# Optimization experiments

Measured on AMD Instinct MI355X. Metric: run time of the kernel, lower is better.

Reference implementation:

```python
import jax, jax.numpy as jnp
import numpy as np

N, S, Q, P = 20000, 400, 20, 3


def setup_inputs() -> dict:
    key = jax.random.key(0)
    k1, k2, k3, k4 = jax.random.split(key, 4)
    # Learned parameters (post-projection state: non-negative, ~L2-normalized)
    heads_param = jax.random.uniform(k1, (S, Q, P), dtype=jnp.float32)
    heads_param = heads_param / jnp.linalg.norm(heads_param, axis=-1, keepdims=True)
    head_ratios_param = jax.random.uniform(k2, (S,), dtype=jnp.float32)
    head_ratios_param = head_ratios_param / jnp.linalg.norm(head_ratios_param)
    # Forward inputs
    batch_pauli_tensor = jax.random.uniform(k3, (N, Q, P), dtype=jnp.float32)
    batch_coeff = jax.random.normal(k4, (N,), dtype=jnp.float32)
    return {
        "heads_param": heads_param,
        "head_ratios_param": head_ratios_param,
        "batch_pauli_tensor": batch_pauli_tensor,
        "batch_coeff": batch_coeff,
    }


def reference(heads_param, head_ratios_param, batch_pauli_tensor, batch_coeff):
    p_exp = 2  # module-level constant `p`
    heads = heads_param ** p_exp              # [s,q,p]
    head_ratios = head_ratios_param ** p_exp  # [s]
    # coverage per (word, head, qubit): dot over Pauli axis
    shadow_coverage = jnp.einsum('nqp,sqp->nsq', batch_pauli_tensor, heads)  # [n,s,q]
    coverage = jnp.prod(shadow_coverage, axis=-1)                            # [n,s]
    coverage = jnp.einsum('s,ns->n', head_ratios, coverage)                  # [n]
    loss_val = jnp.sum((batch_coeff ** 2) / coverage)
    return (loss_val, head_ratios, heads)
```

## Files before the change

### kernel.cpp

```cpp
#include <hip/hip_runtime.h>

#define NN 20000
#define SS 400
#define QQ 20
#define PP 3
#define QP (QQ*PP)
#define NPB 64
#define NBLK ((NN + NPB - 1)/NPB)
#define NPAD (NBLK*NPB)

#define GSPLIT 10
#define SPAIRS (SS/2)
#define SP_PER_BLK (SPAIRS/GSPLIT)
#define WAVES 4
#define BLK_B (WAVES*64)
#define SP_PER_WAVE (SP_PER_BLK/WAVES)

#define WS_H    0
#define WS_R    (SPAIRS*QP*2)
#define WS_COV  (WS_R + SS)
#define WS_PART (WS_COV + GSPLIT*NPAD)
#define CBLK    ((NPAD + 255)/256)

typedef float v2f __attribute__((ext_vector_type(2)));

__device__ __forceinline__ v2f lo4(float4 f) { v2f r; r.x = f.x; r.y = f.y; return r; }
__device__ __forceinline__ v2f hi4(float4 f) { v2f r; r.x = f.z; r.y = f.w; return r; }

__global__ void prep_kernel(const float* __restrict__ heads_param,
                            const float* __restrict__ ratios_param,
                            float* __restrict__ out, float* __restrict__ ws) {
    int i = blockIdx.x * blockDim.x + threadIdx.x;
    if (i < SS*QP) {
        float v = heads_param[i];
        float v2 = v * v;
        out[1 + SS + i] = v2;
        int s = i / QP;
        int k = i - s * QP;
        int sp = s >> 1, j = s & 1;
        ws[WS_H + (sp*QP + k)*2 + j] = v2;
    }
    if (i < SS) {
        float v = ratios_param[i];
        float v2 = v * v;
        out[1 + i] = v2;
        ws[WS_R + i] = v2;
    }
}

#define SP_STEP(ACC, SP)                                                \
    do {                                                                \
        const float4* row4 = lds_h4 + (wbase + (SP))*30 + c*6;          \
        float4 f0 = row4[0], f1 = row4[1], f2 = row4[2];                \
        v2f d0 = lo4(f0)*pqa.x + hi4(f0)*pqa.y + lo4(f1)*pqa.z;         \
        v2f d1 = hi4(f1)*pqa.w + lo4(f2)*pqb.x + hi4(f2)*pqb.y;         \
        float4 f3 = row4[3], f4 = row4[4], f5 = row4[5];                \
        v2f d2 = lo4(f3)*pqb.z + hi4(f3)*pqb.w + lo4(f4)*pqc.x;         \
        v2f d3 = hi4(f4)*pqc.y + lo4(f5)*pqc.z + hi4(f5)*pqc.w;         \
        ACC *= (d0*d1)*(d2*d3);                                         \
    } while (0)

__global__ __launch_bounds__(BLK_B) void main_kernel(
        const float* __restrict__ pauli, float* __restrict__ ws) {
    __shared__ float4 lds_h4[SP_PER_BLK * QP / 2];
    __shared__ float4 lds_r4[SP_PER_BLK * 2 / 4];
    __shared__ float  lds_cov[WAVES][NPB];

    const int tid  = threadIdx.x;
    const int wave = __builtin_amdgcn_readfirstlane(tid >> 6);
    const int lane = tid & 63;
    const int g    = blockIdx.y;
    const int n    = blockIdx.x * NPB + lane;
    const int nc   = (n < NN) ? n : (NN - 1);
    const int wbase = wave * SP_PER_WAVE;

    {
        const float4* srcH = reinterpret_cast<const float4*>(ws + WS_H + (size_t)g * (SP_PER_BLK*QP*2));
        for (int i = tid; i < SP_PER_BLK*QP/2; i += BLK_B) lds_h4[i] = srcH[i];
        const float4* srcR = reinterpret_cast<const float4*>(ws + WS_R + g * (SP_PER_BLK*2));
        if (tid < SP_PER_BLK*2/4) lds_r4[tid] = srcR[tid];
    }

    const float4* p4 = reinterpret_cast<const float4*>(pauli + (size_t)nc * QP);

    __syncthreads();

    v2f a0, a1, a2, a3, a4;
    a0.x=1.f; a0.y=1.f; a1=a0; a2=a0; a3=a0; a4=a0;

    #pragma unroll 1
    for (int c = 0; c < 5; ++c) {
        float4 pqa = p4[c*3+0], pqb = p4[c*3+1], pqc = p4[c*3+2];
        SP_STEP(a0, 0);
        SP_STEP(a1, 1);
        SP_STEP(a2, 2);
        SP_STEP(a3, 3);
        SP_STEP(a4, 4);
    }

    const v2f* r2p = reinterpret_cast<const v2f*>(lds_r4);
    v2f cov2 = r2p[wbase+0]*a0 + r2p[wbase+1]*a1 + r2p[wbase+2]*a2
             + r2p[wbase+3]*a3 + r2p[wbase+4]*a4;

    lds_cov[wave][lane] = cov2.x + cov2.y;
    __syncthreads();

    if (tid < NPB) {
        float cv = 0.f;
        #pragma unroll
        for (int w = 0; w < WAVES; ++w) cv += lds_cov[w][tid];
        ws[WS_COV + (size_t)g * NPAD + blockIdx.x * NPB + tid] = cv;
    }
}

__global__ void combine_kernel(const float* __restrict__ wsc,
                               const float* __restrict__ coeff,
                               float* __restrict__ ws) {
    __shared__ float red[4];
    const int tid = threadIdx.x;
    const int n = blockIdx.x * 256 + tid;
    float term = 0.f;
    if (n < NN) {
        float cov = 0.f;
        #pragma unroll
        for (int g = 0; g < GSPLIT; ++g) cov += wsc[WS_COV + (size_t)g * NPAD + n];
        float c = coeff[n];
        term = (c * c) / cov;
    }
    #pragma unroll
    for (int off = 32; off; off >>= 1) term += __shfl_down(term, off);
    if ((tid & 63) == 0) red[tid >> 6] = term;
    __syncthreads();
    if (tid == 0) ws[WS_PART + blockIdx.x] = red[0] + red[1] + red[2] + red[3];
}

__global__ void final_kernel(const float* __restrict__ ws, float* __restrict__ out) {
    int tid = threadIdx.x;
    double acc = 0.0;
    for (int i = tid; i < CBLK; i += 128) acc += (double)ws[WS_PART + i];
    #pragma unroll
    for (int off = 32; off; off >>= 1) acc += __shfl_down(acc, off);
    __shared__ double r2[2];
    if ((tid & 63) == 0) r2[tid >> 6] = acc;
    __syncthreads();
    if (tid == 0) out[0] = (float)(r2[0] + r2[1]);
}

extern "C" void kernel_launch(void* const* d_in, const int* in_sizes, int n_in,
                              void* d_out, int out_size, void* d_ws, size_t ws_size,
                              hipStream_t stream) {
    const float* heads_param  = (const float*)d_in[0];
    const float* ratios_param = (const float*)d_in[1];
    const float* pauli        = (const float*)d_in[2];
    const float* coeff        = (const float*)d_in[3];
    float* out = (float*)d_out;
    float* ws  = (float*)d_ws;

    prep_kernel<<<(SS*QP + 255)/256, 256, 0, stream>>>(heads_param, ratios_param, out, ws);
    main_kernel<<<dim3(NBLK, GSPLIT), BLK_B, 0, stream>>>(pauli, ws);
    combine_kernel<<<CBLK, 256, 0, stream>>>(ws, coeff, ws);
    final_kernel<<<1, 128, 0, stream>>>(ws, out);
}
```

Measured before the change: 34.82 us.

## Pack word pairs into vector lanes and fold head ratios into heads

The prep kernel now interleaves the Pauli tensor so that each lane processes two words at once as a float2, with heads stored unpacked and read as broadcast scalars. The head ratio is folded into the first qubit's head entries, so the per-head weighting step is replaced by a plain sum. Waves per block are doubled so each wave still covers five heads. The cost is an extra full read and write of the Pauli tensor in the prep kernel, which may outweigh the savings in the main kernel.

```diff
diff --git a/kernel.cpp b/kernel.cpp
--- a/kernel.cpp
+++ b/kernel.cpp
@@ -3,24 +3,23 @@
 #define NN 20000
 #define SS 400
 #define QQ 20
-#define PP 3
-#define QP (QQ*PP)
-#define NPB 64
-#define NBLK ((NN + NPB - 1)/NPB)
-#define NPAD (NBLK*NPB)
-
+#define QP 60
+#define NPAIRS ((NN+1)/2)
+#define JPB 64
+#define NBLK ((NPAIRS + JPB - 1)/JPB)
+#define JPAD (NBLK*JPB)
+#define NP2 (JPAD*2)
 #define GSPLIT 10
-#define SPAIRS (SS/2)
-#define SP_PER_BLK (SPAIRS/GSPLIT)
-#define WAVES 4
+#define SB (SS/GSPLIT)
+#define WAVES 8
 #define BLK_B (WAVES*64)
-#define SP_PER_WAVE (SP_PER_BLK/WAVES)
+#define SW (SB/WAVES)
 
 #define WS_H    0
-#define WS_R    (SPAIRS*QP*2)
-#define WS_COV  (WS_R + SS)
-#define WS_PART (WS_COV + GSPLIT*NPAD)
-#define CBLK    ((NPAD + 255)/256)
+#define WS_P    (SS*QP)
+#define WS_COV  (WS_P + JPAD*QP*2)
+#define WS_PART (WS_COV + GSPLIT*NP2)
+#define CBLK    ((NP2 + 255)/256)
 
 typedef float v2f __attribute__((ext_vector_type(2)));
 
@@ -29,87 +28,85 @@
 
 __global__ void prep_kernel(const float* __restrict__ heads_param,
                             const float* __restrict__ ratios_param,
+                            const float* __restrict__ pauli,
                             float* __restrict__ out, float* __restrict__ ws) {
     int i = blockIdx.x * blockDim.x + threadIdx.x;
+    if (i < NN*QP) {
+        int n = i / QP, k = i - n * QP;
+        int j = n >> 1, b = n & 1;
+        ws[WS_P + j*(QP*2) + k*2 + b] = pauli[i];
+    }
     if (i < SS*QP) {
+        int s = i / QP, k = i - s * QP;
         float v = heads_param[i];
         float v2 = v * v;
         out[1 + SS + i] = v2;
-        int s = i / QP;
-        int k = i - s * QP;
-        int sp = s >> 1, j = s & 1;
-        ws[WS_H + (sp*QP + k)*2 + j] = v2;
+        float r = ratios_param[s];
+        ws[WS_H + i] = (k < 3) ? v2 * (r*r) : v2;
     }
     if (i < SS) {
-        float v = ratios_param[i];
-        float v2 = v * v;
-        out[1 + i] = v2;
-        ws[WS_R + i] = v2;
+        float r = ratios_param[i];
+        out[1 + i] = r * r;
     }
 }
 
-#define SP_STEP(ACC, SP)                                                \
+#define S_STEP(A, S)                                                    \
     do {                                                                \
-        const float4* row4 = lds_h4 + (wbase + (SP))*30 + c*6;          \
-        float4 f0 = row4[0], f1 = row4[1], f2 = row4[2];                \
-        v2f d0 = lo4(f0)*pqa.x + hi4(f0)*pqa.y + lo4(f1)*pqa.z;         \
-        v2f d1 = hi4(f1)*pqa.w + lo4(f2)*pqb.x + hi4(f2)*pqb.y;         \
-        float4 f3 = row4[3], f4 = row4[4], f5 = row4[5];                \
-        v2f d2 = lo4(f3)*pqb.z + hi4(f3)*pqb.w + lo4(f4)*pqc.x;         \
-        v2f d3 = hi4(f4)*pqc.y + lo4(f5)*pqc.z + hi4(f5)*pqc.w;         \
-        ACC *= (d0*d1)*(d2*d3);                                         \
+        const float4* hf = reinterpret_cast<const float4*>(hw + (S)*QP + c*12); \
+        float4 f0 = hf[0], f1 = hf[1], f2 = hf[2];                      \
+        v2f d0 = pq0*f0.x + pq1*f0.y  + pq2*f0.z;                       \
+        v2f d1 = pq3*f0.w + pq4*f1.x  + pq5*f1.y;                       \
+        v2f d2 = pq6*f1.z + pq7*f1.w  + pq8*f2.x;                       \
+        v2f d3 = pq9*f2.y + pq10*f2.z + pq11*f2.w;                      \
+        A *= (d0*d1)*(d2*d3);                                           \
     } while (0)
 
-__global__ __launch_bounds__(BLK_B) void main_kernel(
-        const float* __restrict__ pauli, float* __restrict__ ws) {
-    __shared__ float4 lds_h4[SP_PER_BLK * QP / 2];
-    __shared__ float4 lds_r4[SP_PER_BLK * 2 / 4];
-    __shared__ float  lds_cov[WAVES][NPB];
+__global__ __launch_bounds__(BLK_B) void main_kernel(float* __restrict__ ws) {
+    __shared__ float ldsH[SB*QP];
+    __shared__ v2f   ldsC[WAVES][64];
 
     const int tid  = threadIdx.x;
     const int wave = __builtin_amdgcn_readfirstlane(tid >> 6);
     const int lane = tid & 63;
     const int g    = blockIdx.y;
-    const int n    = blockIdx.x * NPB + lane;
-    const int nc   = (n < NN) ? n : (NN - 1);
-    const int wbase = wave * SP_PER_WAVE;
+    const int j    = blockIdx.x * JPB + lane;
 
     {
-        const float4* srcH = reinterpret_cast<const float4*>(ws + WS_H + (size_t)g * (SP_PER_BLK*QP*2));
-        for (int i = tid; i < SP_PER_BLK*QP/2; i += BLK_B) lds_h4[i] = srcH[i];
-        const float4* srcR = reinterpret_cast<const float4*>(ws + WS_R + g * (SP_PER_BLK*2));
-        if (tid < SP_PER_BLK*2/4) lds_r4[tid] = srcR[tid];
+        const float4* src = reinterpret_cast<const float4*>(ws + WS_H + (size_t)g * (SB*QP));
+        float4* dst = reinterpret_cast<float4*>(ldsH);
+        for (int i = tid; i < SB*QP/4; i += BLK_B) dst[i] = src[i];
     }
-
-    const float4* p4 = reinterpret_cast<const float4*>(pauli + (size_t)nc * QP);
-
     __syncthreads();
 
+    const float4* ppj = reinterpret_cast<const float4*>(ws + WS_P + (size_t)j * (QP*2));
+    const float* hw = ldsH + wave * (SW*QP);
+
     v2f a0, a1, a2, a3, a4;
-    a0.x=1.f; a0.y=1.f; a1=a0; a2=a0; a3=a0; a4=a0;
+    a0.x = 1.f; a0.y = 1.f; a1 = a0; a2 = a0; a3 = a0; a4 = a0;
 
     #pragma unroll 1
     for (int c = 0; c < 5; ++c) {
-        float4 pqa = p4[c*3+0], pqb = p4[c*3+1], pqc = p4[c*3+2];
-        SP_STEP(a0, 0);
-        SP_STEP(a1, 1);
-        SP_STEP(a2, 2);
-        SP_STEP(a3, 3);
-        SP_STEP(a4, 4);
+        float4 q0 = ppj[c*6+0], q1 = ppj[c*6+1], q2 = ppj[c*6+2];
+        float4 q3 = ppj[c*6+3], q4 = ppj[c*6+4], q5 = ppj[c*6+5];
+        v2f pq0 = lo4(q0), pq1  = hi4(q0), pq2  = lo4(q1), pq3  = hi4(q1);
+        v2f pq4 = lo4(q2), pq5  = hi4(q2), pq6  = lo4(q3), pq7  = hi4(q3);
+        v2f pq8 = lo4(q4), pq9  = hi4(q4), pq10 = lo4(q5), pq11 = hi4(q5);
+        S_STEP(a0, 0);
+        S_STEP(a1, 1);
+        S_STEP(a2, 2);
+        S_STEP(a3, 3);
+        S_STEP(a4, 4);
     }
 
-    const v2f* r2p = reinterpret_cast<const v2f*>(lds_r4);
-    v2f cov2 = r2p[wbase+0]*a0 + r2p[wbase+1]*a1 + r2p[wbase+2]*a2
-             + r2p[wbase+3]*a3 + r2p[wbase+4]*a4;
-
-    lds_cov[wave][lane] = cov2.x + cov2.y;
+    v2f cv = ((a0 + a1) + (a2 + a3)) + a4;
+    ldsC[wave][lane] = cv;
     __syncthreads();
 
-    if (tid < NPB) {
-        float cv = 0.f;
+    if (wave == 0) {
+        v2f t = ldsC[0][lane];
         #pragma unroll
-        for (int w = 0; w < WAVES; ++w) cv += lds_cov[w][tid];
-        ws[WS_COV + (size_t)g * NPAD + blockIdx.x * NPB + tid] = cv;
+        for (int w = 1; w < WAVES; ++w) t += ldsC[w][lane];
+        *reinterpret_cast<v2f*>(ws + WS_COV + (size_t)g * NP2 + 2*j) = t;
     }
 }
 
@@ -123,7 +120,7 @@
     if (n < NN) {
         float cov = 0.f;
         #pragma unroll
-        for (int g = 0; g < GSPLIT; ++g) cov += wsc[WS_COV + (size_t)g * NPAD + n];
+        for (int g = 0; g < GSPLIT; ++g) cov += wsc[WS_COV + (size_t)g * NP2 + n];
         float c = coeff[n];
         term = (c * c) / cov;
     }
@@ -156,8 +153,8 @@
     float* out = (float*)d_out;
     float* ws  = (float*)d_ws;
 
-    prep_kernel<<<(SS*QP + 255)/256, 256, 0, stream>>>(heads_param, ratios_param, out, ws);
-    main_kernel<<<dim3(NBLK, GSPLIT), BLK_B, 0, stream>>>(pauli, ws);
+    prep_kernel<<<(NN*QP + 255)/256, 256, 0, stream>>>(heads_param, ratios_param, pauli, out, ws);
+    main_kernel<<<dim3(NBLK, GSPLIT), BLK_B, 0, stream>>>(ws);
     combine_kernel<<<CBLK, 256, 0, stream>>>(ws, coeff, ws);
     final_kernel<<<1, 128, 0, stream>>>(ws, out);
 }
```

Measured after the change: 45.60 us. 31.0% more time.
